# Optimization experiments

Hardware: AMD Instinct MI355X
Metric: run time of the kernel (lower is better)

The kernel has to match this reference:

```python
import jax, jax.numpy as jnp
import numpy as np
import math
from functools import partial

PAD_IDX = 0
EPS = 1e-5  # torch LayerNorm default
H = 8       # num_heads

def _layernorm(x, g, b):
    m = x.mean(-1, keepdims=True)
    v = ((x - m) ** 2).mean(-1, keepdims=True)  # biased var, as torch LN
    return (x - m) / jnp.sqrt(v + EPS) * g + b

def setup_inputs() -> dict:
    key = jax.random.key(0)
    V, D, F, L, B, T = 32000, 512, 2048, 6, 8, 2048
    ks = jax.random.split(key, 24)
    n = lambda k, s: jax.random.normal(k, s, jnp.float32) * 0.02
    x = jax.random.randint(ks[0], (B, T), 1, V)
    x = x.at[:B // 2, -64:].set(PAD_IDX)  # padded tails to exercise mask
    embed = n(ks[1], (V, D)).at[PAD_IDX].set(0.0)  # padding_idx row is zero
    pos = np.arange(T)[:, None].astype(np.float32)
    div = np.exp(np.arange(0, D, 2).astype(np.float32) * (-math.log(10000.0) / D))
    pe = np.zeros((T, D), np.float32)
    pe[:, 0::2] = np.sin(pos * div)
    pe[:, 1::2] = np.cos(pos * div)
    # per-layer params stacked on leading L axis; Linear weights stored [in, out]
    return {
        'x': x, 'embed': embed, 'pe': jnp.asarray(pe),
        'Wq': n(ks[2], (L, D, D)), 'bq': jnp.zeros((L, D)),
        'Wk': n(ks[3], (L, D, D)), 'bk': jnp.zeros((L, D)),
        'Wv': n(ks[4], (L, D, D)), 'bv': jnp.zeros((L, D)),
        'Wo': n(ks[5], (L, D, D)), 'bo': jnp.zeros((L, D)),
        'ln1_g': jnp.ones((L, D)), 'ln1_b': jnp.zeros((L, D)),
        'W1': n(ks[6], (L, D, F)), 'b1': jnp.zeros((L, F)),
        'W2': n(ks[7], (L, F, D)), 'b2': jnp.zeros((L, D)),
        'ln2_g': jnp.ones((L, D)), 'ln2_b': jnp.zeros((L, D)),
        'sent_W': n(ks[8], (D, 3)), 'sent_b': jnp.zeros((3,)),
        'len_W': n(ks[9], (D, 3)), 'len_b': jnp.zeros((3,)),
    }

def reference(x, embed, pe, Wq, bq, Wk, bk, Wv, bv, Wo, bo, ln1_g, ln1_b,
              W1, b1, W2, b2, ln2_g, ln2_b, sent_W, sent_b, len_W, len_b):
    B, T = x.shape
    D = embed.shape[1]
    dk = D // H
    mask = (x == PAD_IDX)  # [B,T], True at pad keys
    h = embed[x] + pe[:T]  # [B,T,D]

    def block(h, p):
        wq, bq_, wk, bk_, wv, bv_, wo, bo_, g1, gb1, w1, fb1, w2, fb2, g2, gb2 = p
        q = (h @ wq + bq_).reshape(B, T, H, dk)
        k = (h @ wk + bk_).reshape(B, T, H, dk)
        v = (h @ wv + bv_).reshape(B, T, H, dk)
        scores = jnp.einsum('bqhd,bkhd->bhqk', q, k) / math.sqrt(dk)  # [B,H,T,T]
        scores = jnp.where(mask[:, None, None, :], -jnp.inf, scores)
        attn = jax.nn.softmax(scores, axis=-1)
        o = jnp.einsum('bhqk,bkhd->bqhd', attn, v).reshape(B, T, D) @ wo + bo_
        h = _layernorm(h + o, g1, gb1)
        ff = jax.nn.relu(h @ w1 + fb1) @ w2 + fb2
        h = _layernorm(h + ff, g2, gb2)
        return h, None

    params = (Wq, bq, Wk, bk, Wv, bv, Wo, bo, ln1_g, ln1_b, W1, b1, W2, b2, ln2_g, ln2_b)
    h, _ = jax.lax.scan(block, h, params)
    cls = h[:, 0, :]
    return (cls @ sent_W + sent_b, cls @ len_W + len_b, cls)
```

## Files before the change

### kernel.cpp

```cpp
#include <hip/hip_runtime.h>
#include <hip/hip_bf16.h>

typedef __bf16 bf16x8 __attribute__((ext_vector_type(8)));
typedef float f32x4 __attribute__((ext_vector_type(4)));
typedef float f32x16 __attribute__((ext_vector_type(16)));
typedef short s16x8 __attribute__((ext_vector_type(8)));
typedef unsigned u32x4 __attribute__((ext_vector_type(4)));

#define LOG2E 1.44269504088896f

__device__ __forceinline__ void gll16(const void* g, void* l) {
  __builtin_amdgcn_global_load_lds((const __attribute__((address_space(1))) void*)g,
                                   (__attribute__((address_space(3))) void*)l, 16, 0, 0);
}

__device__ __forceinline__ unsigned cvt_pk_bf16(float lo, float hi_) {
  unsigned r;
  asm("v_cvt_pk_bf16_f32 %0, %1, %2" : "=v"(r) : "v"(lo), "v"(hi_));
  return r;
}
__device__ __forceinline__ void pswap(unsigned& a, unsigned& b) {
  asm("v_permlane32_swap_b32 %0, %1" : "+v"(a), "+v"(b));
}

__device__ __forceinline__ int swzv(int row, int cbyte) {
  return (row * 128 + cbyte) ^ (((row >> 3) & 7) << 4);
}

__global__ __launch_bounds__(256)
void wtrans_kernel(const float* __restrict__ in, __hip_bfloat16* __restrict__ out,
                   int K, int N, size_t lstride_in, size_t lstride_out) {
  __shared__ float tile[64][65];
  const size_t mi = (size_t)blockIdx.z * lstride_in;
  const size_t mo = (size_t)blockIdx.z * lstride_out;
  const int k0 = blockIdx.x * 64, n0 = blockIdx.y * 64;
  const int t = threadIdx.x;
  const int r = t >> 4, c = (t & 15) * 4;
#pragma unroll
  for (int it = 0; it < 4; ++it) {
    const float4 v = *(const float4*)&in[mi + (size_t)(k0 + it * 16 + r) * N + n0 + c];
    tile[it * 16 + r][c + 0] = v.x; tile[it * 16 + r][c + 1] = v.y;
    tile[it * 16 + r][c + 2] = v.z; tile[it * 16 + r][c + 3] = v.w;
  }
  __syncthreads();
#pragma unroll
  for (int it = 0; it < 4; ++it) {
    const int n = it * 16 + r;
    __hip_bfloat16 hb[4];
#pragma unroll
    for (int j = 0; j < 4; ++j) hb[j] = __float2bfloat16(tile[c + j][n]);
    *(uint2*)&out[mo + (size_t)(n0 + n) * K + k0 + c] = *(uint2*)hb;
  }
}

__global__ void kbias_kernel(const int* __restrict__ x, float* __restrict__ kb) {
  const int i = blockIdx.x * 256 + threadIdx.x;
  kb[i] = (x[i] == 0) ? -1e30f : 0.f;
}

__global__ void tmask_kernel(const int* __restrict__ x, unsigned* __restrict__ tm) {
  const int tid = threadIdx.x;
  const int w = tid >> 6, lane = tid & 63;
  const int b = w * 2 + (lane >> 5), kt = lane & 31;
  int all64 = 1, any = 0;
  for (int i = 0; i < 64; ++i) {
    const int v = (x[b * 2048 + kt * 64 + i] == 0);
    any |= v; all64 &= v;
  }
  const unsigned long long bf = __ballot(all64);
  const unsigned long long bp = __ballot(any && !all64);
  if (lane == 0) { tm[(w * 2) * 2] = (unsigned)bf; tm[(w * 2) * 2 + 1] = (unsigned)bp; }
  if (lane == 32) { tm[(w * 2 + 1) * 2] = (unsigned)(bf >> 32); tm[(w * 2 + 1) * 2 + 1] = (unsigned)(bp >> 32); }
}

__global__ void bcat_kernel(const float* __restrict__ bq, const float* __restrict__ bk,
                            const float* __restrict__ bv, float* __restrict__ o) {
  const int l = blockIdx.x, t = threadIdx.x;
  o[l * 1536 + t] = bq[l * 512 + t];
  o[l * 1536 + 512 + t] = bk[l * 512 + t];
  o[l * 1536 + 1024 + t] = bv[l * 512 + t];
}

__global__ __launch_bounds__(128)
void embed_kernel(const int* __restrict__ x, const float* __restrict__ emb,
                  const float* __restrict__ pe, float* __restrict__ h32,
                  __hip_bfloat16* __restrict__ hbf) {
  const int row = blockIdx.x;
  const int t = row & 2047;
  const int tok = x[row];
  const int d = threadIdx.x * 4;
  const float4 e = *(const float4*)&emb[(size_t)tok * 512 + d];
  const float4 p = *(const float4*)&pe[(size_t)t * 512 + d];
  float4 rv; rv.x = e.x + p.x; rv.y = e.y + p.y; rv.z = e.z + p.z; rv.w = e.w + p.w;
  *(float4*)&h32[(size_t)row * 512 + d] = rv;
  __hip_bfloat16 hb[4] = {__float2bfloat16(rv.x), __float2bfloat16(rv.y),
                          __float2bfloat16(rv.z), __float2bfloat16(rv.w)};
  *(uint2*)&hbf[(size_t)row * 512 + d] = *(uint2*)hb;
}

template <bool RELU>
__global__ __launch_bounds__(256)
void gemm_kernel(const __hip_bfloat16* __restrict__ A, const __hip_bfloat16* __restrict__ Bt,
                 const float* __restrict__ bias, __hip_bfloat16* __restrict__ Cb,
                 int M, int N, int K) {
  constexpr int BK = 32;
  __shared__ __hip_bfloat16 Ash[2][128 * BK];
  __shared__ __hip_bfloat16 Bsh[2][128 * BK];
  const int m0 = blockIdx.x * 128, n0 = blockIdx.y * 128;
  const int tid = threadIdx.x;
  const int lane = tid & 63, wid = tid >> 6;
  const int wr = wid >> 1, wc = wid & 1;
  const int cl = lane & 15, gr = lane >> 4;

  const int ar = tid >> 2;
  const int ac = (tid & 3) << 3;
  const __hip_bfloat16* Ag = A + (size_t)(m0 + ar) * K + ac;
  const __hip_bfloat16* Bg = Bt + (size_t)(n0 + ar) * K + ac;
  const int ldst = tid * 8;

  f32x4 acc[4][4] = {};
  const int KT = K / BK;

  auto stage = [&](int buf, int kt) {
    const size_t ko = (size_t)kt * BK;
    gll16(Ag + ko, &Ash[buf][ldst]);
    gll16(Ag + ko + (size_t)64 * K, &Ash[buf][2048 + ldst]);
    gll16(Bg + ko, &Bsh[buf][ldst]);
    gll16(Bg + ko + (size_t)64 * K, &Bsh[buf][2048 + ldst]);
  };

  stage(0, 0);
  __syncthreads();
  int cur = 0;
  for (int kt = 0; kt < KT; ++kt) {
    if (kt + 1 < KT) stage(cur ^ 1, kt + 1);
    bf16x8 aF[4], bF[4];
#pragma unroll
    for (int i = 0; i < 4; ++i) {
      aF[i] = *(const bf16x8*)&Ash[cur][(wr * 64 + i * 16 + cl) * BK + gr * 8];
      bF[i] = *(const bf16x8*)&Bsh[cur][(wc * 64 + i * 16 + cl) * BK + gr * 8];
    }
#pragma unroll
    for (int i = 0; i < 4; ++i)
#pragma unroll
      for (int j = 0; j < 4; ++j)
        acc[i][j] = __builtin_amdgcn_mfma_f32_16x16x32_bf16(aF[i], bF[j], acc[i][j], 0, 0, 0);
    __syncthreads();
    cur ^= 1;
  }

  float bv[4];
#pragma unroll
  for (int j = 0; j < 4; ++j) bv[j] = bias[n0 + wc * 64 + j * 16 + cl];
#pragma unroll
  for (int i = 0; i < 4; ++i) {
    const int rowb = m0 + wr * 64 + i * 16 + gr * 4;
#pragma unroll
    for (int rr = 0; rr < 4; ++rr) {
      const size_t ro = (size_t)(rowb + rr) * N;
#pragma unroll
      for (int j = 0; j < 4; ++j) {
        float v = acc[i][j][rr] + bv[j];
        if (RELU) v = v > 0.f ? v : 0.f;
        const int col = n0 + wc * 64 + j * 16 + cl;
        Cb[ro + col] = __float2bfloat16(v);
      }
    }
  }
}

__global__ __launch_bounds__(256)
void vtrans_kernel(const __hip_bfloat16* __restrict__ qkv, __hip_bfloat16* __restrict__ vt) {
  constexpr int T = 2048, QS = 1536;
  __shared__ __hip_bfloat16 tile[64 * 64];
  const int tt = blockIdx.x, bh = blockIdx.y;
  const int b = bh >> 3, h = bh & 7;
  const int tid = threadIdx.x;
  const int r = tid >> 2, c0 = (tid & 3) * 16;
  const __hip_bfloat16* src = qkv + ((size_t)(b * T + tt * 64 + r)) * QS + 1024 + h * 64 + c0;
  *(bf16x8*)((char*)tile + swzv(r, c0 * 2)) = *(const bf16x8*)src;
  *(bf16x8*)((char*)tile + swzv(r, c0 * 2 + 16)) = *(const bf16x8*)(src + 8);
  __syncthreads();
  __hip_bfloat16 buf[16];
#pragma unroll
  for (int j = 0; j < 16; ++j)
    buf[j] = *(__hip_bfloat16*)((char*)tile + swzv(c0 + j, r * 2));
  __hip_bfloat16* dst = vt + ((size_t)(bh * 64 + r)) * T + tt * 64 + c0;
  *(uint4*)dst = ((uint4*)buf)[0];
  *(uint4*)(dst + 8) = ((uint4*)buf)[1];
}

__global__ __launch_bounds__(512, 4)
void attn5_kernel(const __hip_bfloat16* __restrict__ qkv, const __hip_bfloat16* __restrict__ Vt,
                  const float* __restrict__ kbias, const unsigned* __restrict__ tmaskg,
                  __hip_bfloat16* __restrict__ Og) {
  constexpr int T = 2048, NT = T / 64, QS = 1536;
  __shared__ __hip_bfloat16 Ks[2][64 * 64];
  __shared__ __hip_bfloat16 Vs[2][64 * 64];
  __shared__ float bc[8][32];
  const int bid = blockIdx.x;
  const int wg = (bid & 7) * 64 + (bid >> 3);
  const int qb = wg & 7, bh = wg >> 3;
  const int b = bh >> 3, h = bh & 7;
  const int tid = threadIdx.x;
  const int w = tid >> 6, lane = tid & 63;
  const int col = lane & 31, hi = lane >> 5;
  const unsigned fullm = tmaskg[b * 2], partm = tmaskg[b * 2 + 1];

  const int sr = tid >> 3;
  const int sc = 8 * ((tid & 7) ^ (sr & 7));
  const __hip_bfloat16* kp = qkv + ((size_t)(b * T + sr)) * QS + 512 + h * 64 + sc;
  const __hip_bfloat16* vp = Vt + ((size_t)(bh * 64 + sr)) * T + sc;

  auto stage = [&](int buf, int kt) {
    gll16(kp + (size_t)kt * 64 * QS, (char*)Ks[buf] + tid * 16);
    gll16(vp + kt * 64, (char*)Vs[buf] + tid * 16);
  };

  const float qscale = 0.125f * LOG2E;
  s16x8 qf[4];
  {
    const __hip_bfloat16* qptr =
        qkv + ((size_t)(b * T + qb * 256 + w * 32 + col)) * QS + h * 64 + 8 * hi;
#pragma unroll
    for (int ks = 0; ks < 4; ++ks) {
      s16x8 raw = *(const s16x8*)(qptr + ks * 16);
#pragma unroll
      for (int j = 0; j < 8; ++j) {
        const unsigned u = ((unsigned)(unsigned short)raw[j]) << 16;
        const float f = __uint_as_float(u) * qscale;
        const __hip_bfloat16 hb = __float2bfloat16(f);
        raw[j] = *(const short*)&hb;
      }
      qf[ks] = raw;
    }
  }

  stage(0, 0);
  __syncthreads();

  f32x16 o0 = {}, o1 = {}, lacc = {};

  for (int kt = 0; kt < NT; ++kt) {
    const int cur = kt & 1;
    if (kt + 1 < NT) stage(cur ^ 1, kt + 1);

    if (!((fullm >> kt) & 1)) {
      f32x16 s0 = {}, s1 = {};
      {
        const char* kbase = (const char*)Ks[cur];
        __builtin_amdgcn_s_setprio(1);
#pragma unroll
        for (int ks = 0; ks < 4; ++ks) {
          const int sl = ((2 * ks + hi) ^ (col & 7)) * 16;
          const bf16x8 k0 = *(const bf16x8*)(kbase + col * 128 + sl);
          const bf16x8 k1 = *(const bf16x8*)(kbase + 4096 + col * 128 + sl);
          const bf16x8 q8 = *(const bf16x8*)&qf[ks];
          s0 = __builtin_amdgcn_mfma_f32_32x32x16_bf16(k0, q8, s0, 0, 0, 0);
          s1 = __builtin_amdgcn_mfma_f32_32x32x16_bf16(k1, q8, s1, 0, 0, 0);
        }
        __builtin_amdgcn_s_setprio(0);
      }

      if ((partm >> kt) & 1) {
        const float* kbp = kbias + (size_t)b * T + kt * 64;
#pragma unroll
        for (int r = 0; r < 16; ++r) {
          const int k16 = (r & 3) + 8 * (r >> 2) + 4 * hi;
          s0[r] += kbp[k16];
          s1[r] += kbp[32 + k16];
        }
      }

#pragma unroll
      for (int r = 0; r < 16; ++r) {
        s0[r] = __builtin_amdgcn_exp2f(s0[r]);
        s1[r] = __builtin_amdgcn_exp2f(s1[r]);
        lacc[r] += s0[r] + s1[r];
      }

      {
        const char* vbase = (const char*)Vs[cur];
#pragma unroll
        for (int kb2 = 0; kb2 < 2; ++kb2) {
          const f32x16& sv = kb2 ? s1 : s0;
#pragma unroll
          for (int half = 0; half < 2; ++half) {
            const int ks = kb2 * 2 + half;
            const int rb = half * 8;
            unsigned wa = cvt_pk_bf16(sv[rb + 0], sv[rb + 1]);
            unsigned wb = cvt_pk_bf16(sv[rb + 2], sv[rb + 3]);
            unsigned wc = cvt_pk_bf16(sv[rb + 4], sv[rb + 5]);
            unsigned wd = cvt_pk_bf16(sv[rb + 6], sv[rb + 7]);
            pswap(wa, wc);
            pswap(wb, wd);
            const u32x4 paw = {wa, wb, wc, wd};
            const bf16x8 pa = __builtin_bit_cast(bf16x8, paw);
            const int sl = ((2 * ks + hi) ^ (col & 7)) * 16;
            const bf16x8 v0 = *(const bf16x8*)(vbase + col * 128 + sl);
            const bf16x8 v1 = *(const bf16x8*)(vbase + 4096 + col * 128 + sl);
            __builtin_amdgcn_s_setprio(1);
            o0 = __builtin_amdgcn_mfma_f32_32x32x16_bf16(pa, v0, o0, 0, 0, 0);
            o1 = __builtin_amdgcn_mfma_f32_32x32x16_bf16(pa, v1, o1, 0, 0, 0);
            __builtin_amdgcn_s_setprio(0);
          }
        }
      }
    }
    __syncthreads();
  }

  float sm[16];
#pragma unroll
  for (int r = 0; r < 16; ++r) sm[r] = lacc[r];
#pragma unroll
  for (int st = 8; st >= 1; st >>= 1)
#pragma unroll
    for (int r = 0; r < st; ++r) sm[r] += sm[r + st];
  const float lrun = sm[0] + __shfl_xor(sm[0], 32);

  bc[w][col] = 1.f / lrun;
  __hip_bfloat16* op = Og + ((size_t)(b * T + qb * 256 + w * 32)) * 512 + h * 64;
#pragma unroll
  for (int r = 0; r < 16; ++r) {
    const int query = (r & 3) + 8 * (r >> 2) + 4 * hi;
    const float li = bc[w][query];
    op[(size_t)query * 512 + col] = __float2bfloat16(o0[r] * li);
    op[(size_t)query * 512 + 32 + col] = __float2bfloat16(o1[r] * li);
  }
}

__global__ __launch_bounds__(128)
void add_ln_kernel(const float* hin, const __hip_bfloat16* __restrict__ proj,
                   const float* __restrict__ g, const float* __restrict__ be,
                   float* hout, __hip_bfloat16* __restrict__ hbf) {
  const int row = blockIdx.x;
  const int tid = threadIdx.x;
  const int d = tid * 4;
  __shared__ float red[4];
  const size_t off = (size_t)row * 512 + d;
  float4 a = *(const float4*)&hin[off];
  const uint2 pu = *(const uint2*)&proj[off];
  const __hip_bfloat16* ph = (const __hip_bfloat16*)&pu;
  a.x += __bfloat162float(ph[0]); a.y += __bfloat162float(ph[1]);
  a.z += __bfloat162float(ph[2]); a.w += __bfloat162float(ph[3]);
  float s = a.x + a.y + a.z + a.w;
  float q = a.x * a.x + a.y * a.y + a.z * a.z + a.w * a.w;
#pragma unroll
  for (int o2 = 1; o2 < 64; o2 <<= 1) {
    s += __shfl_xor(s, o2);
    q += __shfl_xor(q, o2);
  }
  const int w = tid >> 6;
  if ((tid & 63) == 0) { red[w * 2] = s; red[w * 2 + 1] = q; }
  __syncthreads();
  s = red[0] + red[2]; q = red[1] + red[3];
  const float mean = s * (1.f / 512.f);
  const float var = q * (1.f / 512.f) - mean * mean;
  const float rstd = rsqrtf(var + 1e-5f);
  const float4 gg = *(const float4*)&g[d];
  const float4 bb = *(const float4*)&be[d];
  float4 y;
  y.x = (a.x - mean) * rstd * gg.x + bb.x;
  y.y = (a.y - mean) * rstd * gg.y + bb.y;
  y.z = (a.z - mean) * rstd * gg.z + bb.z;
  y.w = (a.w - mean) * rstd * gg.w + bb.w;
  *(float4*)&hout[off] = y;
  __hip_bfloat16 hb[4] = {__float2bfloat16(y.x), __float2bfloat16(y.y),
                          __float2bfloat16(y.z), __float2bfloat16(y.w)};
  *(uint2*)&hbf[off] = *(uint2*)hb;
}

__global__ __launch_bounds__(256)
void head_kernel(const float* __restrict__ h32, const float* __restrict__ sW,
                 const float* __restrict__ sb, const float* __restrict__ lW,
                 const float* __restrict__ lb, float* __restrict__ out) {
  const int tid = threadIdx.x;
  for (int i = tid; i < 4096; i += 256) {
    const int bb = i >> 9, d = i & 511;
    out[48 + i] = h32[(size_t)bb * 2048 * 512 + d];
  }
  if (tid < 192) {
    const int g = tid >> 2, s4 = tid & 3;
    const int which = g / 24, rem = g % 24;
    const int bb = rem / 3, j = rem % 3;
    const float* W = which ? lW : sW;
    const float* bias = which ? lb : sb;
    const float* cls = h32 + (size_t)bb * 2048 * 512;
    float acc = 0.f;
    for (int d = s4; d < 512; d += 4) acc += cls[d] * W[d * 3 + j];
    acc += __shfl_xor(acc, 1);
    acc += __shfl_xor(acc, 2);
    if (s4 == 0) out[which * 24 + bb * 3 + j] = acc + bias[j];
  }
}

extern "C" void kernel_launch(void* const* d_in, const int* in_sizes, int n_in,
                              void* d_out, int out_size, void* d_ws, size_t ws_size,
                              hipStream_t stream) {
  (void)in_sizes; (void)n_in; (void)out_size; (void)ws_size;
  const int* x = (const int*)d_in[0];
  const float* embed = (const float*)d_in[1];
  const float* pe = (const float*)d_in[2];
  const float* Wq = (const float*)d_in[3];
  const float* bq = (const float*)d_in[4];
  const float* Wk = (const float*)d_in[5];
  const float* bk = (const float*)d_in[6];
  const float* Wv = (const float*)d_in[7];
  const float* bvv = (const float*)d_in[8];
  const float* Wo = (const float*)d_in[9];
  const float* bo = (const float*)d_in[10];
  const float* ln1g = (const float*)d_in[11];
  const float* ln1b = (const float*)d_in[12];
  const float* W1 = (const float*)d_in[13];
  const float* b1 = (const float*)d_in[14];
  const float* W2 = (const float*)d_in[15];
  const float* b2 = (const float*)d_in[16];
  const float* ln2g = (const float*)d_in[17];
  const float* ln2b = (const float*)d_in[18];
  const float* sW = (const float*)d_in[19];
  const float* sb = (const float*)d_in[20];
  const float* lW = (const float*)d_in[21];
  const float* lb = (const float*)d_in[22];
  float* out = (float*)d_out;

  constexpr int L = 6, Dm = 512, F = 2048, B = 8, T = 2048;
  constexpr int M = B * T;
  constexpr int QS = 1536;

  char* w = (char*)d_ws;
  auto alloc = [&](size_t bytes) {
    char* p = w; w += (bytes + 255) & ~(size_t)255; return p;
  };
  __hip_bfloat16* wqkvt = (__hip_bfloat16*)alloc((size_t)L * QS * Dm * 2);
  __hip_bfloat16* wot = (__hip_bfloat16*)alloc((size_t)L * Dm * Dm * 2);
  __hip_bfloat16* w1t = (__hip_bfloat16*)alloc((size_t)L * Dm * F * 2);
  __hip_bfloat16* w2t = (__hip_bfloat16*)alloc((size_t)L * Dm * F * 2);
  float* bqkv = (float*)alloc((size_t)L * QS * 4);
  float* h32 = (float*)alloc((size_t)M * Dm * 4);
  __hip_bfloat16* hbf = (__hip_bfloat16*)alloc((size_t)M * Dm * 2);
  char* regionA = alloc((size_t)M * F * 2);
  __hip_bfloat16* vtg = (__hip_bfloat16*)regionA;
  __hip_bfloat16* attno = (__hip_bfloat16*)(regionA + (size_t)M * Dm * 2);
  __hip_bfloat16* ffn1 = (__hip_bfloat16*)regionA;
  char* regionB = alloc((size_t)M * QS * 2);
  __hip_bfloat16* qkvb = (__hip_bfloat16*)regionB;
  __hip_bfloat16* tmpb = (__hip_bfloat16*)regionB;
  float* kbias = (float*)alloc((size_t)M * 4);
  unsigned* tmask = (unsigned*)alloc(64);

  const size_t DD = (size_t)Dm * Dm;
  wtrans_kernel<<<dim3(8, 8, L), 256, 0, stream>>>(Wq, wqkvt, Dm, Dm, DD, (size_t)QS * Dm);
  wtrans_kernel<<<dim3(8, 8, L), 256, 0, stream>>>(Wk, wqkvt + DD, Dm, Dm, DD, (size_t)QS * Dm);
  wtrans_kernel<<<dim3(8, 8, L), 256, 0, stream>>>(Wv, wqkvt + 2 * DD, Dm, Dm, DD, (size_t)QS * Dm);
  wtrans_kernel<<<dim3(8, 8, L), 256, 0, stream>>>(Wo, wot, Dm, Dm, DD, DD);
  wtrans_kernel<<<dim3(8, 32, L), 256, 0, stream>>>(W1, w1t, Dm, F, (size_t)Dm * F, (size_t)Dm * F);
  wtrans_kernel<<<dim3(32, 8, L), 256, 0, stream>>>(W2, w2t, F, Dm, (size_t)Dm * F, (size_t)Dm * F);
  bcat_kernel<<<L, 512, 0, stream>>>(bq, bk, bvv, bqkv);
  kbias_kernel<<<M / 256, 256, 0, stream>>>(x, kbias);
  tmask_kernel<<<1, 256, 0, stream>>>(x, tmask);
  embed_kernel<<<M, 128, 0, stream>>>(x, embed, pe, h32, hbf);

  for (int l = 0; l < L; ++l) {
    const __hip_bfloat16* wqkv_ = wqkvt + (size_t)l * QS * Dm;
    const __hip_bfloat16* wo_ = wot + (size_t)l * Dm * Dm;
    const __hip_bfloat16* w1_ = w1t + (size_t)l * Dm * F;
    const __hip_bfloat16* w2_ = w2t + (size_t)l * Dm * F;

    gemm_kernel<false><<<dim3(128, 12), 256, 0, stream>>>(hbf, wqkv_, bqkv + l * QS, qkvb, M, QS, Dm);
    vtrans_kernel<<<dim3(32, 64), 256, 0, stream>>>(qkvb, vtg);
    attn5_kernel<<<512, 512, 0, stream>>>(qkvb, vtg, kbias, tmask, attno);
    gemm_kernel<false><<<dim3(128, 4), 256, 0, stream>>>(attno, wo_, bo + l * Dm, tmpb, M, Dm, Dm);
    add_ln_kernel<<<M, 128, 0, stream>>>(h32, tmpb, ln1g + l * Dm, ln1b + l * Dm, h32, hbf);
    gemm_kernel<true><<<dim3(128, 16), 256, 0, stream>>>(hbf, w1_, b1 + l * F, ffn1, M, F, Dm);
    gemm_kernel<false><<<dim3(128, 4), 256, 0, stream>>>(ffn1, w2_, b2 + l * Dm, tmpb, M, Dm, F);
    add_ln_kernel<<<M, 128, 0, stream>>>(h32, tmpb, ln2g + l * Dm, ln2b + l * Dm, h32, hbf);
  }
  head_kernel<<<1, 256, 0, stream>>>(h32, sW, sb, lW, lb, out);
}
```

Before: 1.731 ms.

## Split attention key range across two half-workgroups and merge partial sums

The attention kernel now runs 1024 threads per workgroup. Each 512-thread half processes 16 of the 32 key tiles into its own double-buffered LDS region, and the two partial outputs and row sums are combined through shared memory before normalisation and store. This doubles the number of waves working on each query block, to improve latency hiding and occupancy, at the cost of an LDS reduction step and more LDS per workgroup. The GEMM kernel also gets a min-blocks launch bound of 4, which may constrain register allocation.

```diff
diff --git a/kernel.cpp b/kernel.cpp
--- a/kernel.cpp
+++ b/kernel.cpp
@@ -3,6 +3,7 @@
 
 typedef __bf16 bf16x8 __attribute__((ext_vector_type(8)));
 typedef float f32x4 __attribute__((ext_vector_type(4)));
+typedef float f32x8 __attribute__((ext_vector_type(8)));
 typedef float f32x16 __attribute__((ext_vector_type(16)));
 typedef short s16x8 __attribute__((ext_vector_type(8)));
 typedef unsigned u32x4 __attribute__((ext_vector_type(4)));
@@ -99,7 +100,7 @@
 }
 
 template <bool RELU>
-__global__ __launch_bounds__(256)
+__global__ __launch_bounds__(256, 4)
 void gemm_kernel(const __hip_bfloat16* __restrict__ A, const __hip_bfloat16* __restrict__ Bt,
                  const float* __restrict__ bias, __hip_bfloat16* __restrict__ Cb,
                  int M, int N, int K) {
@@ -190,38 +191,44 @@
   *(uint4*)(dst + 8) = ((uint4*)buf)[1];
 }
 
-__global__ __launch_bounds__(512, 4)
-void attn5_kernel(const __hip_bfloat16* __restrict__ qkv, const __hip_bfloat16* __restrict__ Vt,
+__global__ __launch_bounds__(1024, 8)
+void attn7_kernel(const __hip_bfloat16* __restrict__ qkv, const __hip_bfloat16* __restrict__ Vt,
                   const float* __restrict__ kbias, const unsigned* __restrict__ tmaskg,
-                  __hip_bfloat16* __restrict__ Og) {
-  constexpr int T = 2048, NT = T / 64, QS = 1536;
-  __shared__ __hip_bfloat16 Ks[2][64 * 64];
-  __shared__ __hip_bfloat16 Vs[2][64 * 64];
-  __shared__ float bc[8][32];
+                  __hip_bfloat16* __restrict__ attno) {
+  constexpr int T = 2048, QS = 1536;
+  __shared__ char smem[65536];
+  __shared__ float bcast[8][32];
+  __shared__ float lsum[8][32];
   const int bid = blockIdx.x;
   const int wg = (bid & 7) * 64 + (bid >> 3);
   const int qb = wg & 7, bh = wg >> 3;
   const int b = bh >> 3, h = bh & 7;
   const int tid = threadIdx.x;
-  const int w = tid >> 6, lane = tid & 63;
+  const int split = tid >> 9;
+  const int tid2 = tid & 511;
+  const int w2 = tid2 >> 6, lane = tid2 & 63;
   const int col = lane & 31, hi = lane >> 5;
   const unsigned fullm = tmaskg[b * 2], partm = tmaskg[b * 2 + 1];
-
-  const int sr = tid >> 3;
-  const int sc = 8 * ((tid & 7) ^ (sr & 7));
+  const int kt0 = split * 16;
+
+  char* Kb = smem + split * 16384;
+  char* Vb = smem + 32768 + split * 16384;
+
+  const int sr = tid2 >> 3;
+  const int sc = 8 * ((tid2 & 7) ^ (sr & 7));
   const __hip_bfloat16* kp = qkv + ((size_t)(b * T + sr)) * QS + 512 + h * 64 + sc;
   const __hip_bfloat16* vp = Vt + ((size_t)(bh * 64 + sr)) * T + sc;
 
   auto stage = [&](int buf, int kt) {
-    gll16(kp + (size_t)kt * 64 * QS, (char*)Ks[buf] + tid * 16);
-    gll16(vp + kt * 64, (char*)Vs[buf] + tid * 16);
+    gll16(kp + (size_t)kt * 64 * QS, Kb + buf * 8192 + tid2 * 16);
+    gll16(vp + kt * 64, Vb + buf * 8192 + tid2 * 16);
   };
 
   const float qscale = 0.125f * LOG2E;
   s16x8 qf[4];
   {
     const __hip_bfloat16* qptr =
-        qkv + ((size_t)(b * T + qb * 256 + w * 32 + col)) * QS + h * 64 + 8 * hi;
+        qkv + ((size_t)(b * T + qb * 256 + w2 * 32 + col)) * QS + h * 64 + 8 * hi;
 #pragma unroll
     for (int ks = 0; ks < 4; ++ks) {
       s16x8 raw = *(const s16x8*)(qptr + ks * 16);
@@ -236,19 +243,21 @@
     }
   }
 
-  stage(0, 0);
+  stage(0, kt0);
   __syncthreads();
 
-  f32x16 o0 = {}, o1 = {}, lacc = {};
-
-  for (int kt = 0; kt < NT; ++kt) {
-    const int cur = kt & 1;
-    if (kt + 1 < NT) stage(cur ^ 1, kt + 1);
+  f32x16 o0 = {}, o1 = {};
+  f32x8 lacc = {};
+
+  for (int it = 0; it < 16; ++it) {
+    const int kt = kt0 + it;
+    const int cur = it & 1;
+    if (it + 1 < 16) stage(cur ^ 1, kt + 1);
 
     if (!((fullm >> kt) & 1)) {
       f32x16 s0 = {}, s1 = {};
       {
-        const char* kbase = (const char*)Ks[cur];
+        const char* kbase = Kb + cur * 8192;
         __builtin_amdgcn_s_setprio(1);
 #pragma unroll
         for (int ks = 0; ks < 4; ++ks) {
@@ -276,11 +285,11 @@
       for (int r = 0; r < 16; ++r) {
         s0[r] = __builtin_amdgcn_exp2f(s0[r]);
         s1[r] = __builtin_amdgcn_exp2f(s1[r]);
-        lacc[r] += s0[r] + s1[r];
+        lacc[r & 7] += s0[r] + s1[r];
       }
 
       {
-        const char* vbase = (const char*)Vs[cur];
+        const char* vbase = Vb + cur * 8192;
 #pragma unroll
         for (int kb2 = 0; kb2 < 2; ++kb2) {
           const f32x16& sv = kb2 ? s1 : s0;
@@ -310,23 +319,37 @@
     __syncthreads();
   }
 
-  float sm[16];
-#pragma unroll
-  for (int r = 0; r < 16; ++r) sm[r] = lacc[r];
-#pragma unroll
-  for (int st = 8; st >= 1; st >>= 1)
+  float sm[8];
+#pragma unroll
+  for (int r = 0; r < 8; ++r) sm[r] = lacc[r];
+#pragma unroll
+  for (int st = 4; st >= 1; st >>= 1)
 #pragma unroll
     for (int r = 0; r < st; ++r) sm[r] += sm[r + st];
   const float lrun = sm[0] + __shfl_xor(sm[0], 32);
 
-  bc[w][col] = 1.f / lrun;
-  __hip_bfloat16* op = Og + ((size_t)(b * T + qb * 256 + w * 32)) * 512 + h * 64;
-#pragma unroll
-  for (int r = 0; r < 16; ++r) {
-    const int query = (r & 3) + 8 * (r >> 2) + 4 * hi;
-    const float li = bc[w][query];
-    op[(size_t)query * 512 + col] = __float2bfloat16(o0[r] * li);
-    op[(size_t)query * 512 + 32 + col] = __float2bfloat16(o1[r] * li);
+  float* cb = (float*)smem;
+  if (split) {
+    float* dst = cb + (w2 * 64 + lane) * 32;
+#pragma unroll
+    for (int r = 0; r < 16; ++r) { dst[r] = o0[r]; dst[16 + r] = o1[r]; }
+    if (lane < 32) lsum[w2][col] = lrun;
+  }
+  __syncthreads();
+  if (!split) {
+    const float* src = cb + (w2 * 64 + lane) * 32;
+#pragma unroll
+    for (int r = 0; r < 16; ++r) { o0[r] += src[r]; o1[r] += src[16 + r]; }
+    const float ltot = lrun + lsum[w2][col];
+    bcast[w2][col] = 1.f / ltot;
+    __hip_bfloat16* op = attno + ((size_t)(b * T + qb * 256 + w2 * 32)) * 512 + h * 64;
+#pragma unroll
+    for (int r = 0; r < 16; ++r) {
+      const int query = (r & 3) + 8 * (r >> 2) + 4 * hi;
+      const float li = bcast[w2][query];
+      op[(size_t)query * 512 + col] = __float2bfloat16(o0[r] * li);
+      op[(size_t)query * 512 + 32 + col] = __float2bfloat16(o1[r] * li);
+    }
   }
 }
 
@@ -469,7 +492,7 @@
 
     gemm_kernel<false><<<dim3(128, 12), 256, 0, stream>>>(hbf, wqkv_, bqkv + l * QS, qkvb, M, QS, Dm);
     vtrans_kernel<<<dim3(32, 64), 256, 0, stream>>>(qkvb, vtg);
-    attn5_kernel<<<512, 512, 0, stream>>>(qkvb, vtg, kbias, tmask, attno);
+    attn7_kernel<<<512, 1024, 0, stream>>>(qkvb, vtg, kbias, tmask, attno);
     gemm_kernel<false><<<dim3(128, 4), 256, 0, stream>>>(attno, wo_, bo + l * Dm, tmpb, M, Dm, Dm);
     add_ln_kernel<<<M, 128, 0, stream>>>(h32, tmpb, ln1g + l * Dm, ln1b + l * Dm, h32, hbf);
     gemm_kernel<true><<<dim3(128, 16), 256, 0, stream>>>(hbf, w1_, b1 + l * F, ffn1, M, F, Dm);
```

After: 5.678 ms. +227.9%, slower.
